# Kernel tuning notes

Measured on AMD Instinct MI355X. Metric: run time of the kernel, lower is better.

The kernel has to match this reference:

```python
import jax, jax.numpy as jnp
import numpy as np

L = 16          # num_sites
CHI_MAX = 64    # max bond dimension
VOCAB = 128000
TRUNC_EVERY = 10
DT = jnp.float32


def _mps_add(A, B):
    """Direct sum of two MPS (block-diagonal on bonds, boundaries concatenated)."""
    out = []
    for s in range(L):
        a, b = A[s], B[s]
        cla, d, cra = a.shape
        clb, _, crb = b.shape
        if s == 0:
            out.append(jnp.concatenate([a, b], axis=2))          # [1,d,cra+crb]
        elif s == L - 1:
            out.append(jnp.concatenate([a, b], axis=0))          # [cla+clb,d,1]
        else:
            t = jnp.zeros((cla + clb, d, cra + crb), a.dtype)
            t = t.at[:cla, :, :cra].set(a).at[cla:, :, cra:].set(b)
            out.append(t)
    return out


def _truncate(T, chi_max):
    """Left-to-right SVD sweep truncating every bond to <= chi_max."""
    T = list(T)
    for s in range(L - 1):
        cl, d, cr = T[s].shape
        U, S, Vh = jnp.linalg.svd(T[s].reshape(cl * d, cr), full_matrices=False)
        k = min(chi_max, int(S.shape[0]))
        T[s] = U[:, :k].reshape(cl, d, k)
        carry = S[:k, None] * Vh[:k]                              # [k, cr]
        T[s + 1] = jnp.einsum('kl,ldr->kdr', carry, T[s + 1])
    return T


def _forward(cores_hidden, cores_input, head_w, head_b, init_ctx, toks):
    # D=1 MPO core -> per-site 2x2 matrix acting on the physical index
    Wh = cores_hidden[:, 0, :, :, 0]   # [L,2,2]
    Wi = cores_input[:, 0, :, :, 0]    # [L,2,2]
    e0 = jnp.array([1.0, 0.0], DT).reshape(1, 2, 1)
    e1 = jnp.array([0.0, 1.0], DT).reshape(1, 2, 1)
    ctx = [init_ctx[s] for s in range(L)]
    for t, tok in enumerate(toks, start=1):
        bits = [(tok >> i) & 1 for i in range(L)]
        emb = [e1 if b else e0 for b in reversed(bits)]
        # h_{t+1} = W_hidden @ h_t  (+)  W_input @ embed(token)
        h = [jnp.einsum('ij,ljr->lir', Wh[s], ctx[s]) for s in range(L)]
        x = [jnp.einsum('ij,ljr->lir', Wi[s], emb[s]) for s in range(L)]
        ctx = _mps_add(h, x)
        if t % TRUNC_EVERY == 0 and ctx[0].shape[2] > CHI_MAX:
            ctx = _truncate(ctx, CHI_MAX)
    # predict(): mean of middle site over (left bond, phys) -> feature vector
    vec = ctx[L // 2].mean(axis=(0, 1))
    c = vec.shape[0]
    vec = jnp.pad(vec, (0, CHI_MAX - c)) if c < CHI_MAX else vec[:CHI_MAX]
    return head_w @ vec + head_b


def setup_inputs() -> dict:
    key = jax.random.key(0)
    k1, k2, k3, k4, k5, k6 = jax.random.split(key, 6)
    eye = jnp.eye(2, dtype=DT)
    cores_hidden = (0.02 * jax.random.normal(k1, (L, 1, 2, 2, 1), DT)).at[:, 0, :, :, 0].add(eye)
    cores_input = (0.02 * jax.random.normal(k2, (L, 1, 2, 2, 1), DT)).at[:, 0, :, :, 0].add(eye)
    head_w = jax.random.normal(k3, (VOCAB, CHI_MAX), DT) / jnp.sqrt(jnp.float32(CHI_MAX))
    head_b = 0.02 * jax.random.normal(k4, (VOCAB,), DT)
    init_ctx = jax.random.normal(k5, (L, 1, 2, 1), DT)
    token_ids = jax.random.randint(k6, (100,), 0, 65536, dtype=jnp.int32)
    return {"cores_hidden": cores_hidden, "cores_input": cores_input,
            "head_w": head_w, "head_b": head_b,
            "init_ctx": init_ctx, "token_ids": token_ids}


def reference(cores_hidden, cores_input, head_w, head_b, init_ctx, token_ids):
    toks = [int(t) for t in np.asarray(token_ids)]
    return _forward(cores_hidden, cores_input, head_w, head_b, init_ctx, toks)
```

## Files before the change

kernel.cpp:

```cpp
#include <hip/hip_runtime.h>

typedef double rl;
#define NT 256
#define NSV 71
#define LDA 128
#define LDV 72
#define SML 25
#define VOCAB 128000
#define LP 27
#define PB 129

#define EPS32 1.1920928955078125e-7
#define UNFL32 1.17549435e-38

#define O_CAR   0
#define O_COLS  4608
#define O_VEC   4800
#define O_MA    5120
#define O_MBLG  14208
#define O_MU    23552
#define O_MQ    32768
#define O_MVT   41984
#define O_SUB   47168
#define O_SVTB  52352
#define O_U2    57536
#define O_VT2   62720
#define O_QU    67904
#define O_QV    73088
#define O_TB    78272
#define O_D     83456
#define O_E     83528
#define O_TQ    83600
#define O_TP    83672

__device__ double g_ws[84000];

struct LeafCtx {
  rl LVT[26*LP], LU[26*LP];
  rl b1[26], b2[26], b3[26], b4[26];
  rl sc[6];
  int ia[26], ib[26], ic[26];
  int si[12];
};

struct Sh {
  rl d[72], e[72], tq[72], tp[72], rc[72], rs[72];
  rl dsig[72], zz[72], zh[72], sigm[72], vals[72];
  rl ta[72], tb[72];
  int srcU[72], srcVT[72], perm[72];
  int ia[72], ib[72], ic[72];
  int opk[12], opf[12], opa[12], opb[12], opq[12];
  rl sc[8];
  int si[16];
};

__device__ __forceinline__ void wsync(){
  asm volatile("s_waitcnt vmcnt(0) lgkmcnt(0)" ::: "memory");
}

__device__ __forceinline__ rl d_sign(rl a, rl b){ return (b >= 0.0) ? fabs(a) : -fabs(a); }
__device__ __forceinline__ rl dlapy2(rl x, rl y){
  rl ax=fabs(x), ay=fabs(y);
  rl w = ax>ay?ax:ay, z = ax>ay?ay:ax;
  if(z==0.0) return w;
  rl t = z/w; return w*sqrt(1.0+t*t);
}
__device__ void dlartg(rl f, rl g, rl* cs, rl* sn, rl* r){
  if(g==0.0){ *cs=1.0; *sn=0.0; *r=f; }
  else if(f==0.0){ *cs=0.0; *sn=d_sign(1.0,g); *r=fabs(g); }
  else{
    rl dd = sqrt(f*f+g*g);
    *cs = fabs(f)/dd;
    *r  = d_sign(dd, f);
    *sn = g/(*r);
  }
}

__device__ void dlas2(rl f, rl g, rl h, rl* ssmin, rl* ssmax){
  rl fa=fabs(f), ga=fabs(g), ha=fabs(h);
  rl fhmn=fmin(fa,ha), fhmx=fmax(fa,ha);
  if(fhmn==0.0){
    *ssmin=0.0;
    if(fhmx==0.0) *ssmax=ga;
    else { rl mx=fmax(fhmx,ga), mn=fmin(fhmx,ga); rl q=mn/mx; *ssmax=mx*sqrt(1.0+q*q); }
  } else {
    if(ga < fhmx){
      rl as=1.0+fhmn/fhmx, at=(fhmx-fhmn)/fhmx;
      rl au=(ga/fhmx); au=au*au;
      rl c=2.0/(sqrt(as*as+au)+sqrt(at*at+au));
      *ssmin=fhmn*c; *ssmax=fhmx/c;
    } else {
      rl au=fhmx/ga;
      if(au==0.0){ *ssmin=(fhmn*fhmx)/ga; *ssmax=ga; }
      else{
        rl as=1.0+fhmn/fhmx, at=(fhmx-fhmn)/fhmx;
        rl c=1.0/(sqrt(1.0+(as*au)*(as*au))+sqrt(1.0+(at*au)*(at*au)));
        *ssmin=(fhmn*c)*au; *ssmin=*ssmin+*ssmin;
        *ssmax=ga/(c+c);
      }
    }
  }
}

__device__ void dlasv2(rl f, rl g, rl h, rl* ssmin, rl* ssmax, rl* snr, rl* csr, rl* snl, rl* csl){
  rl ft=f, fa=fabs(f), ht=h, ha=fabs(h);
  int pmax=1;
  bool swp = (ha > fa);
  if(swp){ pmax=3; rl t=ft; ft=ht; ht=t; t=fa; fa=ha; ha=t; }
  rl gt=g, ga=fabs(g);
  rl clt=0, crt=0, slt=0, srt=0;
  if(ga==0.0){ *ssmin=ha; *ssmax=fa; clt=1.0; crt=1.0; slt=0.0; srt=0.0; }
  else{
    bool gasmal=true;
    if(ga > fa){
      pmax=2;
      if((fa/ga) < EPS32){
        gasmal=false;
        *ssmax=ga;
        if(ha>1.0) *ssmin=fa/(ga/ha); else *ssmin=(fa/ga)*ha;
        clt=1.0; slt=ht/gt; srt=1.0; crt=ft/gt;
      }
    }
    if(gasmal){
      rl dd=fa-ha;
      rl lv = (dd==fa) ? 1.0 : dd/fa;
      rl mq = gt/ft;
      rl tv = 2.0-lv;
      rl mm = mq*mq, tt = tv*tv;
      rl sv = sqrt(tt+mm);
      rl rv = (lv==0.0) ? fabs(mq) : sqrt(lv*lv+mm);
      rl a = 0.5*(sv+rv);
      *ssmin = ha/a; *ssmax = fa*a;
      rl t3;
      if(mm==0.0){
        if(lv==0.0) t3 = d_sign(2.0, ft)*d_sign(1.0, gt);
        else t3 = gt/d_sign(dd, ft) + mq/tv;
// ... 345 lines not shown

__device__ void leaf_exec(int f, int n, int sqre, int wantU, LeafCtx* lc, Sh* sh, int lane){
  rl* SVTB = g_ws + O_SVTB; rl* SUB = g_ws + O_SUB;
  int np = n + sqre;
  for(int w=lane; w<np*np; w+=64){ int r2=w/np, c=w-r2*np; lc->LVT[r2*LP+c]=SVTB[(f+r2)+(size_t)LDV*(f+c)]; }
  if(wantU) for(int w=lane; w<n*n; w+=64){ int r2=w/n, c=w-r2*n; lc->LU[r2*LP+c]=SUB[(f+r2)+(size_t)LDV*(f+c)]; }
  wsync();
  if(sqre==1){
    if(lane==0){
      rl cs,snv,rv; rl* dd=sh->d+f; rl* ee=sh->e+f;
      for(int i=0;i<n;++i){
        dlartg(dd[i],ee[i],&cs,&snv,&rv);
        dd[i]=rv;
        if(i<n-1){ ee[i]=snv*dd[i+1]; dd[i+1]=cs*dd[i+1]; }
        else ee[i]=0.0;
        lc->b1[i]=cs; lc->b2[i]=snv;
      }
    }
    wsync();
    if(lane<np){
      rl cur = lc->LVT[0*LP+lane];
      for(int j=0;j<n;++j){
        rl cj=lc->b1[j], sj=lc->b2[j];
        rl t=lc->LVT[(j+1)*LP+lane];
        lc->LVT[j*LP+lane] = sj*t + cj*cur;
        cur = cj*t - sj*cur;
      }
      lc->LVT[n*LP+lane] = cur;
    }
    wsync();
    if(lane==0){
      rl cs,snv,rv; rl* dd=sh->d+f; rl* ee=sh->e+f;
      for(int i=0;i<n-1;++i){
        dlartg(dd[i],ee[i],&cs,&snv,&rv);
        dd[i]=rv; ee[i]=snv*dd[i+1]; dd[i+1]=cs*dd[i+1];
        lc->b1[i]=cs; lc->b2[i]=snv;
      }
    }
    wsync();
    if(wantU && lane<n){
      rl cur = lc->LU[lane*LP+0];
      for(int j=0;j<n-1;++j){
        rl cj=lc->b1[j], sj=lc->b2[j];
        rl t=lc->LU[lane*LP+(j+1)];
        lc->LU[lane*LP+j] = sj*t + cj*cur;
        cur = cj*t - sj*cur;
      }
      lc->LU[lane*LP+(n-1)] = cur;
    }
    wsync();
  }
  bdsqr_wave(n, sh->d+f, sh->e+f, np, wantU? n:0, lc, lane);
  for(int w=lane; w<np*np; w+=64){ int r2=w/np, c=w-r2*np; SVTB[(f+r2)+(size_t)LDV*(f+c)]=lc->LVT[r2*LP+c]; }
  if(wantU) for(int w=lane; w<n*n; w+=64){ int r2=w/n, c=w-r2*n; SUB[(f+r2)+(size_t)LDV*(f+c)]=lc->LU[r2*LP+c]; }
}

__device__ void build_ops(int n, Sh* sh, int tid){
  if(tid==0){
    int sf[12], sn2[12], sq[12], sv[12]; int sp=0, no=0;
    sf[0]=0; sn2[0]=n; sq[0]=0; sv[0]=0; sp=1;
    while(sp>0){
      --sp;
      int f=sf[sp], nn=sn2[sp], q=sq[sp], v=sv[sp];
      if(nn<=SML){ sh->opk[no]=0; sh->opf[no]=f; sh->opa[no]=nn; sh->opb[no]=0; sh->opq[no]=q; ++no; }
      else if(v==0){
        int nl=nn/2, nr=nn-nl-1;
        sf[sp]=f; sn2[sp]=nn; sq[sp]=q; sv[sp]=1; ++sp;
        sf[sp]=f+nl+1; sn2[sp]=nr; sq[sp]=q; sv[sp]=0; ++sp;
        sf[sp]=f; sn2[sp]=nl; sq[sp]=1; sv[sp]=0; ++sp;
      } else {
        int nl=nn/2, nr=nn-nl-1;
        sh->opk[no]=1; sh->opf[no]=f; sh->opa[no]=nl; sh->opb[no]=nr; sh->opq[no]=q; ++no;
      }
    }
    int tk[12], tf2[12], ta2[12], tb3[12], tq3[12]; int c=0;
    for(int i=0;i<no;++i) if(sh->opk[i]==0){ tk[c]=0; tf2[c]=sh->opf[i]; ta2[c]=sh->opa[i]; tb3[c]=sh->opb[i]; tq3[c]=sh->opq[i]; ++c; }
    for(int i=0;i<no;++i) if(sh->opk[i]==1){ tk[c]=1; tf2[c]=sh->opf[i]; ta2[c]=sh->opa[i]; tb3[c]=sh->opb[i]; tq3[c]=sh->opq[i]; ++c; }
    for(int i=0;i<no;++i){ sh->opk[i]=tk[i]; sh->opf[i]=tf2[i]; sh->opa[i]=ta2[i]; sh->opb[i]=tb3[i]; sh->opq[i]=tq3[i]; }
    sh->si[6]=no;
  }
  __syncthreads();
}

__device__ void lasd1_merge(int f, int nl, int nr, int sqre, int wantU, rl* QV, Sh* sh, int tid){
  rl* SUB = g_ws + O_SUB; rl* SVTB = g_ws + O_SVTB;
  rl* U2 = g_ws + O_U2; rl* VT2 = g_ws + O_VT2; rl* QU = g_ws + O_QU;
  int n = nl+nr+1, m = n+sqre;
  {
    rl alpha = sh->d[f+nl], beta = sh->e[f+nl];
    if(tid==0){
      sh->sc[0]=alpha; sh->sc[1]=beta;
      sh->vals[0]=0.0;
      sh->zz[0] = alpha*SVTB[(f+nl)+(size_t)LDV*(f+nl)];
      sh->srcU[0]=-1; sh->srcVT[0]=f+nl;
    } else if(tid<n){
      int i=tid;
      if(i<=nl){
        sh->vals[i]=sh->d[f+i-1];
        sh->zz[i]=alpha*SVTB[(f+i-1)+(size_t)LDV*(f+nl)];
        sh->srcU[i]=f+i-1; sh->srcVT[i]=f+i-1;
      } else {
        int j=i-1-nl;
        sh->vals[i]=sh->d[f+nl+1+j];
        sh->zz[i]=beta*SVTB[(f+nl+1+j)+(size_t)LDV*(f+nl+1)];
        sh->srcU[i]=f+nl+1+j; sh->srcVT[i]=f+nl+1+j;
      }
    }
  }
  __syncthreads();
  if(sqre==1){
    if(tid==0){
      rl zM = sh->sc[1]*SVTB[(f+n)+(size_t)LDV*(f+nl+1)];
      rl c,s2,r2;
      dlartg(sh->zz[0], zM, &c, &s2, &r2);
      sh->zz[0]=r2; sh->sc[2]=c; sh->sc[3]=s2;
    }
    __syncthreads();
    rl c=sh->sc[2], s=sh->sc[3];
    int ra=f+nl, rb=f+n;
    for(int k=tid;k<m;k+=NT){
      size_t ci=(size_t)LDV*(f+k);
      rl a=SVTB[ra+ci], b=SVTB[rb+ci];
      SVTB[ra+ci]=c*a+s*b; SVTB[rb+ci]=-s*a+c*b;
    }
  }
  __syncthreads();
  {
    rl lm = (tid<n)? fabs(sh->vals[tid]) : 0.0;
    for(int off=32;off>0;off>>=1) lm = fmax(lm, __shfl_xor(lm,off,64));
    if((tid&63)==0) sh->ta[tid>>6]=lm;
  }
  __syncthreads();
  {
    rl maxd = fmax(fmax(sh->ta[0],sh->ta[1]), fmax(sh->ta[2],sh->ta[3]));
    rl tol = 8.0*EPS32*fmax(maxd, fmax(fabs(sh->sc[0]), fabs(sh->sc[1])));
    if(tid>=1 && tid<n){
      bool ndt = fabs(sh->zz[tid])>tol;
      rl vt = sh->vals[tid];
      int rank=0, Kc=0;
      for(int j=1;j<n;++j){
        bool ndj = fabs(sh->zz[j])>tol;
        if(ndj) ++Kc;
        if(ndj==ndt){
          rl vj=sh->vals[j];
          if(vj<vt || (vj==vt && j<tid)) ++rank;
        }
      }
      int pos = ndt ? (1+rank) : (1+Kc+rank);
      sh->ic[pos]=tid;
    }
    if(tid==0){
      int Kc=0;
      for(int j=1;j<n;++j) if(fabs(sh->zz[j])>tol) ++Kc;
      sh->ic[0]=0;
      sh->si[0]=1+Kc; sh->si[1]=n; sh->si[2]=m; sh->si[3]=f; sh->si[4]=nl;
    }
  }
  __syncthreads();
  int K=sh->si[0], n_=sh->si[1], m_=sh->si[2], f_=sh->si[3], nl_=sh->si[4];
  if(tid<n_){ sh->ta[tid]=sh->vals[tid]; sh->tb[tid]=sh->zz[tid]; sh->ia[tid]=sh->srcU[tid]; sh->ib[tid]=sh->srcVT[tid]; }
  __syncthreads();
  if(tid<n_){
    int p=sh->ic[tid];
    sh->dsig[tid]=sh->ta[p]; sh->zz[tid]=sh->tb[p]; sh->srcU[tid]=sh->ia[p]; sh->srcVT[tid]=sh->ib[p];
  }
  __syncthreads();
  if(tid==0){
    rl rho=0.0; for(int t=0;t<K;++t){ rl zv=sh->zz[t]; rho += zv*zv; }
    sh->sc[4]=rho;
  }
  if(wantU){
    for(int w=tid; w<n_*n_; w+=NT){
      int col=w/n_, row=w-col*n_;
      int su=sh->srcU[col];
      rl v;
      if(su<0) v = (row==nl_) ? 1.0 : 0.0;
      else v = SUB[(f_+row)+(size_t)LDV*su];
      U2[row+(size_t)LDV*col]=v;
    }
  }
  for(int w=tid; w<n_*m_; w+=NT){
    int row=w/m_, col=w-row*m_;
    VT2[row+(size_t)LDV*col] = SVTB[sh->srcVT[row]+(size_t)LDV*(f_+col)];
  }
  __syncthreads();
  rl rho=sh->sc[4];
  for(int j=tid;j<K;j+=NT){
    rl lo=sh->dsig[j];
    rl hi=(j<K-1)? sh->dsig[j+1] : sqrt(sh->dsig[K-1]*sh->dsig[K-1]+rho);
    for(int it=0; it<130; ++it){
      rl mid=0.5*(lo+hi);
      if(mid<=lo || mid>=hi) break;
      rl g=1.0;
      for(int i2=0;i2<K;++i2){
        rl zi=sh->zz[i2];
        g += zi*zi/((sh->dsig[i2]-mid)*(sh->dsig[i2]+mid));
      }
      if(g<0.0) lo=mid; else hi=mid;
    }
    sh->sigm[j]=0.5*(lo+hi);
  }
  __syncthreads();
  for(int i2=tid;i2<K;i2+=NT){
    rl di=sh->dsig[i2];
    rl p=(di - sh->sigm[K-1])*(di + sh->sigm[K-1]);
    for(int j=0;j<i2;++j)
      p *= (di - sh->sigm[j])*(di + sh->sigm[j])/((di - sh->dsig[j])*(di + sh->dsig[j]));
    for(int j=i2;j<K-1;++j)
      p *= (di - sh->sigm[j])*(di + sh->sigm[j])/((di - sh->dsig[j+1])*(di + sh->dsig[j+1]));
    sh->zh[i2] = d_sign(sqrt(fabs(p)), sh->zz[i2]);
  }
  __syncthreads();
  for(int j=tid;j<K;j+=NT){
    rl sj=sh->sigm[j];
    rl nu=0.0, nv=0.0;
    for(int i2=0;i2<K;++i2){
      rl di=sh->dsig[i2];
      rl vv=sh->zh[i2]/((di-sj)*(di+sj));
      QV[i2+(size_t)LDV*j]=vv; nv+=vv*vv;
      if(wantU){
        rl uu=(i2==0)? -1.0 : di*vv;
        QU[i2+(size_t)LDV*j]=uu; nu+=uu*uu;
      }
    }
    nv=1.0/sqrt(nv);
    for(int i2=0;i2<K;++i2) QV[i2+(size_t)LDV*j]*=nv;
    if(wantU){
      nu=1.0/sqrt(nu);
      for(int i2=0;i2<K;++i2) QU[i2+(size_t)LDV*j]*=nu;
    }
  }
  __syncthreads();
  if(tid==0){
    int nd2=n_-K;
    for(int t=0;t<nd2;++t) sh->ia[t]=K+t;
    int ps=K-1, pd=nd2-1;
    int t=0;
    while(t<n_){
      rl vs = (ps>=0)? sh->sigm[ps] : -1.0;
      rl vd = (pd>=0)? sh->dsig[sh->ia[pd]] : -1.0;
      if(vs >= vd){ sh->perm[t]=ps; sh->vals[t]=vs; --ps; }
      else { sh->perm[t]=1000+sh->ia[pd]; sh->vals[t]=vd; --pd; }
      ++t;
    }
  }
  __syncthreads();
  if(tid<n_) sh->d[f_+tid]=sh->vals[tid];
  if(wantU){
    for(int w=tid; w<n_*n_; w+=NT){
      int t=w/n_, row=w-t*n_;
      int src=sh->perm[t];
      rl acc;
      if(src>=1000) acc = U2[row+(size_t)LDV*(src-1000)];
      else{
        const rl* urow = U2 + row;
        const rl* qcol = QU + (size_t)LDV*src;
        rl s=0.0; int i=0;
        for(; i+16<=K; i+=16){
          rl a[16], b[16];
          #pragma unroll
          for(int u=0;u<16;++u){ a[u]=urow[(size_t)LDV*(size_t)(i+u)]; b[u]=qcol[i+u]; }
          #pragma unroll
          for(int u=0;u<16;++u) s += a[u]*b[u];
        }
        for(; i<K; ++i) s += urow[(size_t)LDV*i]*qcol[i];
        acc=s;
      }
      SUB[(f_+row)+(size_t)LDV*(f_+t)] = acc;
    }
  }
  for(int w=tid; w<n_*m_; w+=NT){
    int t=w/m_, col=w-t*m_;
    int src=sh->perm[t];
    rl acc;
    if(src>=1000) acc = VT2[(src-1000)+(size_t)LDV*col];
    else{
      const rl* qcol = QV + (size_t)LDV*src;
      const rl* vcol = VT2 + (size_t)LDV*col;
      rl s=0.0; int i=0;
      for(; i+16<=K; i+=16){
        rl a[16], b[16];
        #pragma unroll
        for(int u=0;u<16;++u){ a[u]=qcol[i+u]; b[u]=vcol[i+u]; }
        #pragma unroll
        for(int u=0;u<16;++u) s += a[u]*b[u];
      }
      for(; i<K; ++i) s += qcol[i]*vcol[i];
      acc=s;
    }
    SVTB[(f_+t)+(size_t)LDV*(f_+col)] = acc;
  }
  __syncthreads();
}

__device__ __forceinline__ void gebd2_upper(rl* A, int ld, int m, int n, Sh* sh, int tid){
  const int lane = tid & 63;
  rl pend_scl = 0.0; int pend_ds = 0;
  for(int i=0;i<n;++i){
    rl ps=0.0;
    for(int r=i+1+lane;r<m;r+=64){ rl vv=A[r+(size_t)ld*i]; ps+=vv*vv; }
    for(int off=32;off>0;off>>=1) ps += __shfl_xor(ps,off,64);
    rl alpha=A[i+(size_t)ld*i];
    rl xn=sqrt(ps);
    rl beta,tau,scl; int ds;
    if(xn==0.0){ tau=0.0; beta=alpha; scl=0.0; ds=0; }
    else{ beta=-d_sign(dlapy2(alpha,xn),alpha); tau=(beta-alpha)/beta; scl=1.0/(alpha-beta); ds=1; }
    if(tid==0){ sh->d[i]=beta; sh->tq[i]=tau; }
    if(tau!=0.0)
      app_left_s(A, ld, i, m, i+1, n, A+(size_t)ld*i, scl, tau, tid);
    if(pend_ds && tid>=128){
      int c = i+1 + (tid-128);
      if(c < n) A[(i-1)+(size_t)ld*c] *= pend_scl;
    }
    __syncthreads();
    if(i<n-1){
      rl ps2=0.0;
      for(int c=i+2+lane;c<n;c+=64){ rl vv=A[i+(size_t)ld*c]; ps2+=vv*vv; }
      for(int off=32;off>0;off>>=1) ps2 += __shfl_xor(ps2,off,64);
      rl alpha2=A[i+(size_t)ld*(i+1)];
      rl xn2=sqrt(ps2);
      rl beta2,tau2,scl2; int ds2;
      if(xn2==0.0){ tau2=0.0; beta2=alpha2; scl2=0.0; ds2=0; }
      else{ beta2=-d_sign(dlapy2(alpha2,xn2),alpha2); tau2=(beta2-alpha2)/beta2; scl2=1.0/(alpha2-beta2); ds2=1; }
      if(tid==0){ sh->e[i]=beta2; sh->tp[i]=tau2; }
      if(tau2!=0.0)
        app_right_s(A, ld, i+1, m, i+1, n, A+i, ld, scl2, tau2, tid);
      if(ds && tid>=128){
        int r = i+1 + (tid-128);
        if(r < m) A[r+(size_t)ld*i] *= scl;
      }
      pend_ds = ds2; pend_scl = scl2;
      __syncthreads();
    } else {
      if(tid==0) sh->tp[i]=0.0;
      __syncthreads();
      if(ds) for(int r=i+1+tid; r<m; r+=NT) A[r+(size_t)ld*(n-1)] *= scl;
      __syncthreads();
    }
  }
}

__device__ __forceinline__ void gebd2_lower(rl* A, int ld, int m, int n, Sh* sh, int tid){
  const int lane = tid & 63;
  rl pend_scl = 0.0; int pend_ds = 0;
  int last_ds = 0; rl last_scl = 0.0;
  for(int i=0;i<m;++i){
    rl ps=0.0;
    for(int c=i+1+lane;c<n;c+=64){ rl vv=A[i+(size_t)ld*c]; ps+=vv*vv; }
    for(int off=32;off>0;off>>=1) ps += __shfl_xor(ps,off,64);
    rl alpha=A[i+(size_t)ld*i];
    rl xn=sqrt(ps);
    rl beta,tau,scl; int ds;
    if(xn==0.0){ tau=0.0; beta=alpha; scl=0.0; ds=0; }
    else{ beta=-d_sign(dlapy2(alpha,xn),alpha); tau=(beta-alpha)/beta; scl=1.0/(alpha-beta); ds=1; }
    if(tid==0){ sh->d[i]=beta; sh->tp[i]=tau; }
    if(tau!=0.0)
      app_right_s(A, ld, i+1, m, i, n, A+i, ld, scl, tau, tid);
    if(pend_ds && tid>=128){
      int r = i+1 + (tid-128);
      if(r < m) A[r+(size_t)ld*(i-1)] *= pend_scl;
    }
    __syncthreads();
    if(i<m-1){
      rl ps2=0.0;
      for(int r=i+2+lane;r<m;r+=64){ rl vv=A[r+(size_t)ld*i]; ps2+=vv*vv; }
      for(int off=32;off>0;off>>=1) ps2 += __shfl_xor(ps2,off,64);
      rl alpha2=A[(i+1)+(size_t)ld*i];
      rl xn2=sqrt(ps2);
      rl beta2,tau2,scl2; int ds2;
      if(xn2==0.0){ tau2=0.0; beta2=alpha2; scl2=0.0; ds2=0; }
      else{ beta2=-d_sign(dlapy2(alpha2,xn2),alpha2); tau2=(beta2-alpha2)/beta2; scl2=1.0/(alpha2-beta2); ds2=1; }
      if(tid==0){ sh->e[i]=beta2; sh->tq[i]=tau2; }
      if(tau2!=0.0)
        app_left_s(A, ld, i+1, m, i+1, n, A+(size_t)ld*i, scl2, tau2, tid);
      if(ds && tid>=128){
        int c = i+1 + (tid-128);
        if(c < n) A[i+(size_t)ld*c] *= scl;
      }
      pend_ds = ds2; pend_scl = scl2;
      __syncthreads();
    } else {
      last_ds = ds; last_scl = scl;
      __syncthreads();
      if(last_ds) for(int c=i+1+tid; c<n; c+=NT) A[(m-1)+(size_t)ld*c] *= last_scl;
      __syncthreads();
    }
  }
}

__device__ __forceinline__ void gelq2(rl* A, int ld, int m, int n, Sh* sh, int tid){
  const int lane = tid & 63;
  rl pend_scl=0.0, pend_beta=0.0; int pend_ds=0;
  for(int i=0;i<m;++i){
    rl ps=0.0;
    for(int c=i+1+lane;c<n;c+=64){ rl vv=A[i+(size_t)ld*c]; ps+=vv*vv; }
    for(int off=32;off>0;off>>=1) ps += __shfl_xor(ps,off,64);
    rl alpha=A[i+(size_t)ld*i];
    rl xn=sqrt(ps);
    rl beta,tau,scl; int ds;
    if(xn==0.0){ tau=0.0; beta=alpha; scl=0.0; ds=0; }
    else{ beta=-d_sign(dlapy2(alpha,xn),alpha); tau=(beta-alpha)/beta; scl=1.0/(alpha-beta); ds=1; }
    if(tid==0) sh->rs[i]=tau;
    if(i<m-1 && tau!=0.0)
      app_right_s(A, ld, i+1, m, i, n, A+i, ld, scl, tau, tid);
    if(i>0 && tid>=128){
      if(pend_ds){ int c = i + (tid-128); if(c<n) A[(i-1)+(size_t)ld*c] *= pend_scl; }
      if(tid==128) A[(i-1)+(size_t)ld*(i-1)] = pend_beta;
    }
    pend_ds=ds; pend_scl=scl; pend_beta=beta;
    __syncthreads();
  }
  if(tid>=128){
    if(pend_ds){ int c = m + (tid-128); if(c<n) A[(m-1)+(size_t)ld*c] *= pend_scl; }
    if(tid==128) A[(m-1)+(size_t)ld*(m-1)] = pend_beta;
  }
  __syncthreads();
}


__global__ __launch_bounds__(NT)
void k_bidiag(const float* __restrict__ ch, const float* __restrict__ ci,
              const float* __restrict__ ictx, const int* __restrict__ tok,
              int s, int m)
{
  __shared__ Sh sh;
  extern __shared__ rl MBL[];
  int tid = threadIdx.x;
  rl* MA = g_ws + O_MA; rl* MQ = g_ws + O_MQ; rl* TB = g_ws + O_TB;
  if(tid==0){
    rl W00=ch[s*4+0], W01=ch[s*4+1], W10=ch[s*4+2], W11=ch[s*4+3];
    rl P00=1,P01=0,P10=0,P11=1;
    for(int mexp=0;mexp<=70;++mexp){
      int j=70-mexp;
      rl v0,v1;
      if(j==0){ v0=ictx[s*2+0]; v1=ictx[s*2+1]; }
      else{
        int b=(tok[j-1]>>(15-s))&1;
        v0=ci[s*4+b]; v1=ci[s*4+2+b];
      }
      g_ws[O_COLS + 0 + 2*j] = P00*v0+P01*v1;
      g_ws[O_COLS + 1 + 2*j] = P10*v0+P11*v1;
      rl n00=W00*P00+W01*P10, n01=W00*P01+W01*P11;
      rl n10=W10*P00+W11*P10, n11=W10*P01+W11*P11;
      P00=n00;P01=n01;P10=n10;P11=n11;
    }
  }
  __syncthreads();
  for(int w=tid; w<m*NSV; w+=NT){
    int j=w/m, r2=w-j*m;
    int l=r2>>1, dd2=r2&1;
    rl cv = g_ws[O_COLS + dd2 + 2*j];
    MA[r2+(size_t)LDA*j] = (s==0)? cv : g_ws[O_CAR + l + 64*j]*cv;
  }
  __syncthreads();
  if(m==128){
    for(int w=tid;w<128*NSV;w+=NT){ int c=w>>7, r2=w&127; MBL[r2+(size_t)PB*c]=MA[r2+(size_t)LDA*c]; }
    __syncthreads();
    gebd2_upper(MBL, PB, 128, NSV, &sh, tid);
    for(int w=tid;w<PB*NSV;w+=NT) g_ws[O_MBLG+w]=MBL[w];
  } else if(m==64){
    for(int w=tid;w<64*NSV;w+=NT){ int c=w>>6, r2=w&63; MBL[r2+(size_t)PB*c]=MA[r2+(size_t)LDA*c]; }
    __syncthreads();
    gebd2_lower(MBL, PB, 64, NSV, &sh, tid);
    for(int w=tid;w<PB*NSV;w+=NT) g_ws[O_MBLG+w]=MBL[w];
  } else {
    for(int w=tid;w<m*NSV;w+=NT){ int c=w/m, r2=w-c*m; MBL[r2+(size_t)PB*c]=MA[r2+(size_t)LDA*c]; }
    __syncthreads();
    gelq2(MBL, PB, m, NSV, &sh, tid);
    for(int w=tid;w<m*NSV;w+=NT){ int c=w/m, r2=w-c*m; MQ[r2+(size_t)LDA*c]=(r2==c)?1.0:0.0; }
    __syncthreads();
    if(tid<m){
      int r=tid;
      for(int j=m-1;j>=0;--j){
        rl tau=sh.rs[j];
        if(tau!=0.0) row_apply(MQ + r + (size_t)LDA*j, LDA, MBL + j + (size_t)PB*(j+1), PB, NSV-j-1, tau);
      }
    }
    __syncthreads();
    for(int w=tid;w<m*m;w+=NT){ int c=w/m, r2=w-c*m; TB[r2+(size_t)LDV*c]=(r2>=c)? MBL[r2+(size_t)PB*c]:0.0; }
    __syncthreads();
    gebd2_upper(TB, LDV, m, m, &sh, tid);
  }
  if(tid<72){
    g_ws[O_D+tid]=sh.d[tid]; g_ws[O_E+tid]=sh.e[tid];
    g_ws[O_TQ+tid]=sh.tq[tid]; g_ws[O_TP+tid]=sh.tp[tid];
  }
}

__global__ __launch_bounds__(NT)
void k_leaf(int s, int m)
{
  __shared__ Sh sh;
  __shared__ LeafCtx lct[4];
  int tid = threadIdx.x;
  if(tid<72){ sh.d[tid]=g_ws[O_D+tid]; sh.e[tid]=g_ws[O_E+tid]; }
  __syncthreads();
  int wantU = (s==8)?1:0;
  int n_eff = (m==128)? NSV : m;
  if(m==64){
    if(tid==0){
      for(int i=0;i<63;++i){
        rl cs,snv,rv;
        dlartg(sh.d[i], sh.e[i], &cs,&snv,&rv);
        sh.d[i]=rv; sh.e[i]=snv*sh.d[i+1]; sh.d[i+1]=cs*sh.d[i+1];
      }
    }
    __syncthreads();
  }
  rl* SUB = g_ws + O_SUB; rl* SVTB = g_ws + O_SVTB;
  for(int w=tid; w<LDV*LDV; w+=NT){
    int c=w/LDV, r2=w-c*LDV; rl v=(r2==c)?1.0:0.0;
    SVTB[w]=v;
    if(wantU) SUB[w]=v;
  }
  __syncthreads();
  if(n_eff<=SML){
    if((tid>>6)==0) leaf_exec(0, n_eff, 0, wantU, &lct[0], &sh, tid&63);
    __syncthreads();
  } else {
    build_ops(n_eff, &sh, tid);
    int no=sh.si[6];
    int o=0;
    while(o<no && sh.opk[o]==0){
      int cnt=1;
      while(o+cnt<no && sh.opk[o+cnt]==0 && cnt<4) ++cnt;
      int wid = tid>>6;
      if(wid<cnt) leaf_exec(sh.opf[o+wid], sh.opa[o+wid], sh.opq[o+wid], wantU, &lct[wid], &sh, tid&63);
      __syncthreads();
      o += cnt;
    }
  }
  if(tid<72){ g_ws[O_D+tid]=sh.d[tid]; g_ws[O_E+tid]=sh.e[tid]; }
}

__global__ __launch_bounds__(NT)
void k_merge(int s, int m)
{
  __shared__ Sh sh;
  __shared__ rl QV[(size_t)LDV*71];
  int tid = threadIdx.x;
  if(tid<72){ sh.d[tid]=g_ws[O_D+tid]; sh.e[tid]=g_ws[O_E+tid]; }
  __syncthreads();
  int wantU = (s==8)?1:0;
  int n_eff = (m==128)? NSV : m;
  if(n_eff>SML){
    build_ops(n_eff, &sh, tid);
    int no=sh.si[6];
    for(int o=0;o<no;++o){
      if(sh.opk[o]==1)
        lasd1_merge(sh.opf[o], sh.opa[o], sh.opb[o], sh.opq[o], wantU, QV, &sh, tid);
    }
  }
  __syncthreads();
  if(tid<72) g_ws[O_D+tid]=sh.d[tid];
}

__global__ __launch_bounds__(NT)
void k_post(const float* __restrict__ ch, int s, int m)
{
  __shared__ Sh sh;
  extern __shared__ rl MBL[];
  int tid = threadIdx.x;
  rl* MU=g_ws+O_MU; rl* MVT=g_ws+O_MVT; rl* MQ=g_ws+O_MQ;
  rl* SUB=g_ws+O_SUB; rl* SVTB=g_ws+O_SVTB; rl* TB=g_ws+O_TB; rl* VT2=g_ws+O_VT2;
  if(tid<72){
    sh.d[tid]=g_ws[O_D+tid];
    sh.tq[tid]=g_ws[O_TQ+tid];
    sh.tp[tid]=g_ws[O_TP+tid];
  }
  __syncthreads();
  int k = (m<64)? m : 64;
  if(m==128){
    if(s==8){
      for(int w=tid;w<128*NSV;w+=NT){ int c=w>>7, r2=w&127; MU[r2+(size_t)LDA*c]=(r2<NSV)? SUB[r2+(size_t)LDV*c]:0.0; }
      for(int w=tid;w<PB*NSV;w+=NT) MBL[w]=g_ws[O_MBLG+w];
      __syncthreads();
      if(tid<NSV){
        int c=tid;
        rl* colb = MU + (size_t)LDA*c;
        for(int i=NSV-1;i>=0;--i){
          rl tau=sh.tq[i];
          if(tau!=0.0) row_apply(colb+i, 1, MBL + (size_t)PB*i + i + 1, 1, 128-i-1, tau);
        }
      }
      __syncthreads();
      if(tid==0){
        rl W00=ch[8*4+0], W01=ch[8*4+1], W10=ch[8*4+2], W11=ch[8*4+3];
        rl P00=1,P01=0,P10=0,P11=1;
        for(int it=0;it<30;++it){
          rl n00=W00*P00+W01*P10, n01=W00*P01+W01*P11;
          rl n10=W10*P00+W11*P10, n11=W10*P01+W11*P11;
          P00=n00;P01=n01;P10=n10;P11=n11;
        }
        sh.sc[0]=P00+P10; sh.sc[1]=P01+P11;
      }
      __syncthreads();
      for(int r2=tid; r2<64; r2+=NT){
        rl acc=0.0;
        for(int l=0;l<64;++l)
          acc += sh.sc[0]*MU[(2*l)+(size_t)LDA*r2] + sh.sc[1]*MU[(2*l+1)+(size_t)LDA*r2];
        g_ws[O_VEC + r2] = acc/188.0;
      }
    } else {
      for(int w=tid;w<LDV*NSV;w+=NT) MVT[w]=SVTB[w];
      for(int w=tid;w<PB*NSV;w+=NT) MBL[w]=g_ws[O_MBLG+w];
      __syncthreads();
      if(tid<NSV){
        int r=tid;
        for(int i=NSV-2;i>=0;--i){
          rl tau=sh.tp[i];
          if(tau!=0.0) row_apply(MVT + r + (size_t)LDV*(i+1), LDV, MBL + i + (size_t)PB*(i+2), PB, NSV-i-2, tau);
        }
      }
      __syncthreads();
      for(int w=tid; w<k*NSV; w+=NT){
        int j=w/k, l=w-j*k;
        g_ws[O_CAR + l + 64*j] = sh.d[l]*MVT[l+(size_t)LDV*j];
      }
    }
  } else if(m==64){
    for(int w=tid;w<64*NSV;w+=NT){ int c=w>>6, r2=w&63; MVT[r2+(size_t)LDV*c]=(c<64)? SVTB[r2+(size_t)LDV*c]:0.0; }
    for(int w=tid;w<PB*NSV;w+=NT) MBL[w]=g_ws[O_MBLG+w];
    __syncthreads();
    if(tid<64){
      int r=tid;
      for(int i=63;i>=0;--i){
        rl tau=sh.tp[i];
        if(tau!=0.0) row_apply(MVT + r + (size_t)LDV*i, LDV, MBL + i + (size_t)PB*(i+1), PB, NSV-i-1, tau);
      }
    }
    __syncthreads();
    for(int w=tid; w<k*NSV; w+=NT){
      int j=w/k, l=w-j*k;
      g_ws[O_CAR + l + 64*j] = sh.d[l]*MVT[l+(size_t)LDV*j];
    }
  } else {
    for(int w=tid;w<m*m;w+=NT){ int c=w/m, r2=w-c*m; VT2[r2+(size_t)LDV*c]=SVTB[r2+(size_t)LDV*c]; }
    __syncthreads();
    if(tid<m){
      int r=tid;
      for(int i=m-2;i>=0;--i){
        rl tau=sh.tp[i];
        if(tau!=0.0) row_apply(VT2 + r + (size_t)LDV*(i+1), LDV, TB + i + (size_t)LDV*(i+2), LDV, m-i-2, tau);
      }
    }
    __syncthreads();
    for(int w=tid;w<m*NSV;w+=NT){
      int c=w/m, r2=w-c*m;
      const rl* vrow = VT2 + r2;
      const rl* qcol = MQ + (size_t)LDA*c;
      rl s2=0.0; int t=0;
      for(; t+16<=m; t+=16){
        rl a[16], b[16];
        #pragma unroll
        for(int u=0;u<16;++u){ a[u]=vrow[(size_t)LDV*(size_t)(t+u)]; b[u]=qcol[t+u]; }
        #pragma unroll
        for(int u=0;u<16;++u) s2 += a[u]*b[u];
      }
      for(; t+4<=m; t+=4){
        rl a0=vrow[(size_t)LDV*t], a1=vrow[(size_t)LDV*(t+1)], a2=vrow[(size_t)LDV*(t+2)], a3=vrow[(size_t)LDV*(t+3)];
        rl b0=qcol[t], b1=qcol[t+1], b2=qcol[t+2], b3=qcol[t+3];
        s2+=a0*b0; s2+=a1*b1; s2+=a2*b2; s2+=a3*b3;
      }
      for(; t<m; ++t) s2 += vrow[(size_t)LDV*t]*qcol[t];
      MVT[r2+(size_t)LDV*c]=s2;
    }
    __syncthreads();
    for(int w=tid; w<k*NSV; w+=NT){
      int j=w/k, l=w-j*k;
      g_ws[O_CAR + l + 64*j] = sh.d[l]*MVT[l+(size_t)LDV*j];
    }
  }
}

__global__ __launch_bounds__(NT)
void head_kernel(const float* __restrict__ hw, const float* __restrict__ hb,
                 float* __restrict__ out)
{
  __shared__ float v[64];
  int tid=threadIdx.x;
  if(tid<64) v[tid]=(float)g_ws[O_VEC + tid];
  __syncthreads();
  int i = blockIdx.x*NT + tid;
  if(i<VOCAB){
    const float4* row = (const float4*)(hw + (size_t)i*64);
    float acc=0.f;
    #pragma unroll
    for(int c4=0;c4<16;++c4){
      float4 r4=row[c4];
      acc += r4.x*v[4*c4] + r4.y*v[4*c4+1] + r4.z*v[4*c4+2] + r4.w*v[4*c4+3];
    }
    out[i]=acc+hb[i];
  }
}

extern "C" void kernel_launch(void* const* d_in, const int* in_sizes, int n_in,
                              void* d_out, int out_size, void* d_ws, size_t ws_size,
                              hipStream_t stream)
{
  const float* ch  = (const float*)d_in[0];
  const float* ci  = (const float*)d_in[1];
  const float* hw  = (const float*)d_in[2];
  const float* hb  = (const float*)d_in[3];
  const float* ict = (const float*)d_in[4];
  const int*   tk  = (const int*)d_in[5];
  (void)d_ws; (void)ws_size; (void)in_sizes; (void)n_in; (void)out_size;

  static const int ms[9] = {2,4,8,16,32,64,128,128,128};
  size_t dynls = (size_t)PB*NSV*sizeof(double);
  for(int s=0;s<9;++s){
    hipLaunchKernelGGL(k_bidiag, dim3(1), dim3(NT), dynls, stream, ch, ci, ict, tk, s, ms[s]);
    hipLaunchKernelGGL(k_leaf,   dim3(1), dim3(NT), 0,     stream, s, ms[s]);
    if(ms[s] >= 32)
      hipLaunchKernelGGL(k_merge, dim3(1), dim3(NT), 0,    stream, s, ms[s]);
    hipLaunchKernelGGL(k_post,   dim3(1), dim3(NT), dynls, stream, ch, s, ms[s]);
  }
  hipLaunchKernelGGL(head_kernel, dim3((VOCAB+NT-1)/NT), dim3(NT), 0, stream,
                     hw, hb, (float*)d_out);
}
```

Measured before the change: 8.123 ms.

## Fuse SVD stage kernels and run sibling divide-and-conquer merges concurrently

Merges the bidiagonalization and leaf-solve kernels into one, and the merge and post-processing kernels into another, so each truncation step needs two launches instead of four and passes less state through global memory. When the merge tree has three merge operations, the two independent sibling merges now run at the same time on two 128-thread halves of the block, using offset shared and workspace regions. The final merge then runs on the full block. The risks are higher shared-memory use per kernel (LeafCtx and QV now live alongside the dynamic buffer) and correctness hazards if the per-half offsets overlap in the U2/VT2/QU workspaces.

```diff
diff --git a/kernel.cpp b/kernel.cpp
--- a/kernel.cpp
+++ b/kernel.cpp
@@ -50,8 +50,8 @@
   int srcU[72], srcVT[72], perm[72];
   int ia[72], ib[72], ic[72];
   int opk[12], opf[12], opa[12], opb[12], opq[12];
-  rl sc[8];
-  int si[16];
+  rl sc[16];
+  int si[24];
 };
 
 __device__ __forceinline__ void wsync(){
@@ -563,179 +563,184 @@
   __syncthreads();
 }
 
-__device__ void lasd1_merge(int f, int nl, int nr, int sqre, int wantU, rl* QV, Sh* sh, int tid){
+__device__ void lasd1_merge2(int f, int nl, int nr, int sqre, int wantU,
+                             rl* QVL, int qofs, int base, Sh* sh, int ltid, int lnt){
   rl* SUB = g_ws + O_SUB; rl* SVTB = g_ws + O_SVTB;
   rl* U2 = g_ws + O_U2; rl* VT2 = g_ws + O_VT2; rl* QU = g_ws + O_QU;
+  rl* sc = sh->sc + (base?8:0);
+  int* si = sh->si + (base?16:0);
   int n = nl+nr+1, m = n+sqre;
   {
     rl alpha = sh->d[f+nl], beta = sh->e[f+nl];
-    if(tid==0){
-      sh->sc[0]=alpha; sh->sc[1]=beta;
-      sh->vals[0]=0.0;
-      sh->zz[0] = alpha*SVTB[(f+nl)+(size_t)LDV*(f+nl)];
-      sh->srcU[0]=-1; sh->srcVT[0]=f+nl;
-    } else if(tid<n){
-      int i=tid;
+    if(ltid==0){
+      sc[0]=alpha; sc[1]=beta;
+      sh->vals[base]=0.0;
+      sh->zz[base] = alpha*SVTB[(f+nl)+(size_t)LDV*(f+nl)];
+      sh->srcU[base]=-1; sh->srcVT[base]=f+nl;
+    } else if(ltid<n){
+      int i=ltid;
       if(i<=nl){
-        sh->vals[i]=sh->d[f+i-1];
-        sh->zz[i]=alpha*SVTB[(f+i-1)+(size_t)LDV*(f+nl)];
-        sh->srcU[i]=f+i-1; sh->srcVT[i]=f+i-1;
+        sh->vals[base+i]=sh->d[f+i-1];
+        sh->zz[base+i]=alpha*SVTB[(f+i-1)+(size_t)LDV*(f+nl)];
+        sh->srcU[base+i]=f+i-1; sh->srcVT[base+i]=f+i-1;
       } else {
         int j=i-1-nl;
-        sh->vals[i]=sh->d[f+nl+1+j];
-        sh->zz[i]=beta*SVTB[(f+nl+1+j)+(size_t)LDV*(f+nl+1)];
-        sh->srcU[i]=f+nl+1+j; sh->srcVT[i]=f+nl+1+j;
-      }
-    }
+        sh->vals[base+i]=sh->d[f+nl+1+j];
+        sh->zz[base+i]=beta*SVTB[(f+nl+1+j)+(size_t)LDV*(f+nl+1)];
+        sh->srcU[base+i]=f+nl+1+j; sh->srcVT[base+i]=f+nl+1+j;
+      }
+    }
+  }
+  __syncthreads();
+  if(ltid==0 && sqre==1){
+    rl zM = sc[1]*SVTB[(f+n)+(size_t)LDV*(f+nl+1)];
+    rl c,s2,r2;
+    dlartg(sh->zz[base], zM, &c, &s2, &r2);
+    sh->zz[base]=r2; sc[2]=c; sc[3]=s2;
   }
   __syncthreads();
   if(sqre==1){
-    if(tid==0){
-      rl zM = sh->sc[1]*SVTB[(f+n)+(size_t)LDV*(f+nl+1)];
-      rl c,s2,r2;
-      dlartg(sh->zz[0], zM, &c, &s2, &r2);
-      sh->zz[0]=r2; sh->sc[2]=c; sh->sc[3]=s2;
-    }
-    __syncthreads();
-    rl c=sh->sc[2], s=sh->sc[3];
+    rl c=sc[2], s=sc[3];
     int ra=f+nl, rb=f+n;
-    for(int k=tid;k<m;k+=NT){
+    for(int k=ltid;k<m;k+=lnt){
       size_t ci=(size_t)LDV*(f+k);
       rl a=SVTB[ra+ci], b=SVTB[rb+ci];
       SVTB[ra+ci]=c*a+s*b; SVTB[rb+ci]=-s*a+c*b;
     }
   }
   __syncthreads();
+  if(ltid==0){
+    rl maxd=0.0; for(int i=0;i<n;++i) maxd=fmax(maxd,fabs(sh->vals[base+i]));
+    rl tol = 8.0*EPS32*fmax(maxd, fmax(fabs(sc[0]), fabs(sc[1])));
+    sc[5]=tol;
+    int Kc=0;
+    for(int j=1;j<n;++j) if(fabs(sh->zz[base+j]) > tol) ++Kc;
+    sh->ic[base]=0;
+    si[0]=1+Kc; si[1]=n; si[2]=m; si[3]=f; si[4]=nl;
+  }
+  __syncthreads();
   {
-    rl lm = (tid<n)? fabs(sh->vals[tid]) : 0.0;
-    for(int off=32;off>0;off>>=1) lm = fmax(lm, __shfl_xor(lm,off,64));
-    if((tid&63)==0) sh->ta[tid>>6]=lm;
-  }
-  __syncthreads();
-  {
-    rl maxd = fmax(fmax(sh->ta[0],sh->ta[1]), fmax(sh->ta[2],sh->ta[3]));
-    rl tol = 8.0*EPS32*fmax(maxd, fmax(fabs(sh->sc[0]), fabs(sh->sc[1])));
-    if(tid>=1 && tid<n){
-      bool ndt = fabs(sh->zz[tid])>tol;
-      rl vt = sh->vals[tid];
+    rl tol=sc[5];
+    if(ltid>=1 && ltid<n){
+      bool ndt = fabs(sh->zz[base+ltid])>tol;
+      rl vt = sh->vals[base+ltid];
       int rank=0, Kc=0;
       for(int j=1;j<n;++j){
-        bool ndj = fabs(sh->zz[j])>tol;
+        bool ndj = fabs(sh->zz[base+j])>tol;
         if(ndj) ++Kc;
         if(ndj==ndt){
-          rl vj=sh->vals[j];
-          if(vj<vt || (vj==vt && j<tid)) ++rank;
+          rl vj=sh->vals[base+j];
+          if(vj<vt || (vj==vt && j<ltid)) ++rank;
         }
       }
       int pos = ndt ? (1+rank) : (1+Kc+rank);
-      sh->ic[pos]=tid;
-    }
-    if(tid==0){
-      int Kc=0;
-      for(int j=1;j<n;++j) if(fabs(sh->zz[j])>tol) ++Kc;
-      sh->ic[0]=0;
-      sh->si[0]=1+Kc; sh->si[1]=n; sh->si[2]=m; sh->si[3]=f; sh->si[4]=nl;
-    }
-  }
-  __syncthreads();
-  int K=sh->si[0], n_=sh->si[1], m_=sh->si[2], f_=sh->si[3], nl_=sh->si[4];
-  if(tid<n_){ sh->ta[tid]=sh->vals[tid]; sh->tb[tid]=sh->zz[tid]; sh->ia[tid]=sh->srcU[tid]; sh->ib[tid]=sh->srcVT[tid]; }
-  __syncthreads();
-  if(tid<n_){
-    int p=sh->ic[tid];
-    sh->dsig[tid]=sh->ta[p]; sh->zz[tid]=sh->tb[p]; sh->srcU[tid]=sh->ia[p]; sh->srcVT[tid]=sh->ib[p];
-  }
-  __syncthreads();
-  if(tid==0){
-    rl rho=0.0; for(int t=0;t<K;++t){ rl zv=sh->zz[t]; rho += zv*zv; }
-    sh->sc[4]=rho;
+      sh->ic[base+pos]=ltid;
+    }
+  }
+  __syncthreads();
+  int K=si[0], n_=si[1], m_=si[2], f_=si[3], nl_=si[4];
+  if(ltid<n_){ sh->ta[base+ltid]=sh->vals[base+ltid]; sh->tb[base+ltid]=sh->zz[base+ltid]; sh->ia[base+ltid]=sh->srcU[base+ltid]; sh->ib[base+ltid]=sh->srcVT[base+ltid]; }
+  __syncthreads();
+  if(ltid<n_){
+    int p=sh->ic[base+ltid];
+    sh->dsig[base+ltid]=sh->ta[base+p]; sh->zz[base+ltid]=sh->tb[base+p]; sh->srcU[base+ltid]=sh->ia[base+p]; sh->srcVT[base+ltid]=sh->ib[base+p];
+  }
+  __syncthreads();
+  if(ltid==0){
+    rl rho=0.0; for(int t=0;t<K;++t){ rl zv=sh->zz[base+t]; rho += zv*zv; }
+    sc[4]=rho;
   }
   if(wantU){
-    for(int w=tid; w<n_*n_; w+=NT){
+    for(int w=ltid; w<n_*n_; w+=lnt){
       int col=w/n_, row=w-col*n_;
-      int su=sh->srcU[col];
+      int su=sh->srcU[base+col];
       rl v;
       if(su<0) v = (row==nl_) ? 1.0 : 0.0;
       else v = SUB[(f_+row)+(size_t)LDV*su];
-      U2[row+(size_t)LDV*col]=v;
-    }
-  }
-  for(int w=tid; w<n_*m_; w+=NT){
+      U2[(base+row)+(size_t)LDV*(base+col)]=v;
+    }
+  }
+  for(int w=ltid; w<n_*m_; w+=lnt){
     int row=w/m_, col=w-row*m_;
-    VT2[row+(size_t)LDV*col] = SVTB[sh->srcVT[row]+(size_t)LDV*(f_+col)];
-  }
-  __syncthreads();
-  rl rho=sh->sc[4];
-  for(int j=tid;j<K;j+=NT){
-    rl lo=sh->dsig[j];
-    rl hi=(j<K-1)? sh->dsig[j+1] : sqrt(sh->dsig[K-1]*sh->dsig[K-1]+rho);
-    for(int it=0; it<130; ++it){
-      rl mid=0.5*(lo+hi);
-      if(mid<=lo || mid>=hi) break;
-      rl g=1.0;
-      for(int i2=0;i2<K;++i2){
-        rl zi=sh->zz[i2];
-        g += zi*zi/((sh->dsig[i2]-mid)*(sh->dsig[i2]+mid));
-      }
-      if(g<0.0) lo=mid; else hi=mid;
-    }
-    sh->sigm[j]=0.5*(lo+hi);
-  }
-  __syncthreads();
-  for(int i2=tid;i2<K;i2+=NT){
-    rl di=sh->dsig[i2];
-    rl p=(di - sh->sigm[K-1])*(di + sh->sigm[K-1]);
+    VT2[(base+row)+(size_t)LDV*(base+col)] = SVTB[sh->srcVT[base+row]+(size_t)LDV*(f_+col)];
+  }
+  __syncthreads();
+  {
+    rl rho=sc[4];
+    if(ltid<K){
+      int j=ltid;
+      rl lo=sh->dsig[base+j];
+      rl hi=(j<K-1)? sh->dsig[base+j+1] : sqrt(sh->dsig[base+K-1]*sh->dsig[base+K-1]+rho);
+      for(int it=0; it<130; ++it){
+        rl mid=0.5*(lo+hi);
+        if(mid<=lo || mid>=hi) break;
+        rl g=1.0;
+        for(int i2=0;i2<K;++i2){
+          rl zi=sh->zz[base+i2];
+          g += zi*zi/((sh->dsig[base+i2]-mid)*(sh->dsig[base+i2]+mid));
+        }
+        if(g<0.0) lo=mid; else hi=mid;
+      }
+      sh->sigm[base+j]=0.5*(lo+hi);
+    }
+  }
+  __syncthreads();
+  if(ltid<K){
+    int i2=ltid;
+    rl di=sh->dsig[base+i2];
+    rl p=(di - sh->sigm[base+K-1])*(di + sh->sigm[base+K-1]);
     for(int j=0;j<i2;++j)
-      p *= (di - sh->sigm[j])*(di + sh->sigm[j])/((di - sh->dsig[j])*(di + sh->dsig[j]));
+      p *= (di - sh->sigm[base+j])*(di + sh->sigm[base+j])/((di - sh->dsig[base+j])*(di + sh->dsig[base+j]));
     for(int j=i2;j<K-1;++j)
-      p *= (di - sh->sigm[j])*(di + sh->sigm[j])/((di - sh->dsig[j+1])*(di + sh->dsig[j+1]));
-    sh->zh[i2] = d_sign(sqrt(fabs(p)), sh->zz[i2]);
-  }
-  __syncthreads();
-  for(int j=tid;j<K;j+=NT){
-    rl sj=sh->sigm[j];
+      p *= (di - sh->sigm[base+j])*(di + sh->sigm[base+j])/((di - sh->dsig[base+j+1])*(di + sh->dsig[base+j+1]));
+    sh->zh[base+i2] = d_sign(sqrt(fabs(p)), sh->zz[base+i2]);
+  }
+  __syncthreads();
+  if(ltid<K){
+    int j=ltid;
+    rl sj=sh->sigm[base+j];
     rl nu=0.0, nv=0.0;
     for(int i2=0;i2<K;++i2){
-      rl di=sh->dsig[i2];
-      rl vv=sh->zh[i2]/((di-sj)*(di+sj));
-      QV[i2+(size_t)LDV*j]=vv; nv+=vv*vv;
+      rl di=sh->dsig[base+i2];
+      rl vv=sh->zh[base+i2]/((di-sj)*(di+sj));
+      QVL[i2+(size_t)LDV*(j+qofs)]=vv; nv+=vv*vv;
       if(wantU){
         rl uu=(i2==0)? -1.0 : di*vv;
-        QU[i2+(size_t)LDV*j]=uu; nu+=uu*uu;
+        QU[i2+(size_t)LDV*(j+qofs)]=uu; nu+=uu*uu;
       }
     }
     nv=1.0/sqrt(nv);
-    for(int i2=0;i2<K;++i2) QV[i2+(size_t)LDV*j]*=nv;
+    for(int i2=0;i2<K;++i2) QVL[i2+(size_t)LDV*(j+qofs)]*=nv;
     if(wantU){
       nu=1.0/sqrt(nu);
-      for(int i2=0;i2<K;++i2) QU[i2+(size_t)LDV*j]*=nu;
-    }
-  }
-  __syncthreads();
-  if(tid==0){
+      for(int i2=0;i2<K;++i2) QU[i2+(size_t)LDV*(j+qofs)]*=nu;
+    }
+  }
+  __syncthreads();
+  if(ltid==0){
     int nd2=n_-K;
-    for(int t=0;t<nd2;++t) sh->ia[t]=K+t;
+    for(int t=0;t<nd2;++t) sh->ia[base+t]=K+t;
     int ps=K-1, pd=nd2-1;
     int t=0;
     while(t<n_){
-      rl vs = (ps>=0)? sh->sigm[ps] : -1.0;
-      rl vd = (pd>=0)? sh->dsig[sh->ia[pd]] : -1.0;
-      if(vs >= vd){ sh->perm[t]=ps; sh->vals[t]=vs; --ps; }
-      else { sh->perm[t]=1000+sh->ia[pd]; sh->vals[t]=vd; --pd; }
+      rl vs = (ps>=0)? sh->sigm[base+ps] : -1.0;
+      rl vd = (pd>=0)? sh->dsig[base+sh->ia[base+pd]] : -1.0;
+      if(vs >= vd){ sh->perm[base+t]=ps; sh->vals[base+t]=vs; --ps; }
+      else { sh->perm[base+t]=1000+sh->ia[base+pd]; sh->vals[base+t]=vd; --pd; }
       ++t;
     }
   }
   __syncthreads();
-  if(tid<n_) sh->d[f_+tid]=sh->vals[tid];
+  if(ltid<n_) sh->d[f_+ltid]=sh->vals[base+ltid];
   if(wantU){
-    for(int w=tid; w<n_*n_; w+=NT){
+    for(int w=ltid; w<n_*n_; w+=lnt){
       int t=w/n_, row=w-t*n_;
-      int src=sh->perm[t];
+      int src=sh->perm[base+t];
       rl acc;
-      if(src>=1000) acc = U2[row+(size_t)LDV*(src-1000)];
+      if(src>=1000) acc = U2[(base+row)+(size_t)LDV*(base+(src-1000))];
       else{
-        const rl* urow = U2 + row;
-        const rl* qcol = QU + (size_t)LDV*src;
+        const rl* urow = U2 + (base+row) + (size_t)LDV*base;
+        const rl* qcol = QU + (size_t)LDV*(src+qofs);
         rl s=0.0; int i=0;
         for(; i+16<=K; i+=16){
           rl a[16], b[16];
@@ -750,14 +755,14 @@
       SUB[(f_+row)+(size_t)LDV*(f_+t)] = acc;
     }
   }
-  for(int w=tid; w<n_*m_; w+=NT){
+  for(int w=ltid; w<n_*m_; w+=lnt){
     int t=w/m_, col=w-t*m_;
-    int src=sh->perm[t];
+    int src=sh->perm[base+t];
     rl acc;
-    if(src>=1000) acc = VT2[(src-1000)+(size_t)LDV*col];
+    if(src>=1000) acc = VT2[(base+(src-1000))+(size_t)LDV*(base+col)];
     else{
-      const rl* qcol = QV + (size_t)LDV*src;
-      const rl* vcol = VT2 + (size_t)LDV*col;
+      const rl* qcol = QVL + (size_t)LDV*(src+qofs);
+      const rl* vcol = VT2 + base + (size_t)LDV*(base+col);
       rl s=0.0; int i=0;
       for(; i+16<=K; i+=16){
         rl a[16], b[16];
@@ -898,13 +903,13 @@
   __syncthreads();
 }
 
-
 __global__ __launch_bounds__(NT)
-void k_bidiag(const float* __restrict__ ch, const float* __restrict__ ci,
-              const float* __restrict__ ictx, const int* __restrict__ tok,
-              int s, int m)
+void k_front(const float* __restrict__ ch, const float* __restrict__ ci,
+             const float* __restrict__ ictx, const int* __restrict__ tok,
+             int s, int m)
 {
   __shared__ Sh sh;
+  __shared__ LeafCtx lct[4];
   extern __shared__ rl MBL[];
   int tid = threadIdx.x;
   rl* MA = g_ws + O_MA; rl* MQ = g_ws + O_MQ; rl* TB = g_ws + O_TB;
@@ -944,6 +949,14 @@
     __syncthreads();
     gebd2_lower(MBL, PB, 64, NSV, &sh, tid);
     for(int w=tid;w<PB*NSV;w+=NT) g_ws[O_MBLG+w]=MBL[w];
+    __syncthreads();
+    if(tid==0){
+      for(int i=0;i<63;++i){
+        rl cs,snv,rv;
+        dlartg(sh.d[i], sh.e[i], &cs,&snv,&rv);
+        sh.d[i]=rv; sh.e[i]=snv*sh.d[i+1]; sh.d[i+1]=cs*sh.d[i+1];
+      }
+    }
   } else {
     for(int w=tid;w<m*NSV;w+=NT){ int c=w/m, r2=w-c*m; MBL[r2+(size_t)PB*c]=MA[r2+(size_t)LDA*c]; }
     __syncthreads();
@@ -962,32 +975,9 @@
     __syncthreads();
     gebd2_upper(TB, LDV, m, m, &sh, tid);
   }
-  if(tid<72){
-    g_ws[O_D+tid]=sh.d[tid]; g_ws[O_E+tid]=sh.e[tid];
-    g_ws[O_TQ+tid]=sh.tq[tid]; g_ws[O_TP+tid]=sh.tp[tid];
-  }
-}
-
-__global__ __launch_bounds__(NT)
-void k_leaf(int s, int m)
-{
-  __shared__ Sh sh;
-  __shared__ LeafCtx lct[4];
-  int tid = threadIdx.x;
-  if(tid<72){ sh.d[tid]=g_ws[O_D+tid]; sh.e[tid]=g_ws[O_E+tid]; }
   __syncthreads();
   int wantU = (s==8)?1:0;
   int n_eff = (m==128)? NSV : m;
-  if(m==64){
-    if(tid==0){
-      for(int i=0;i<63;++i){
-        rl cs,snv,rv;
-        dlartg(sh.d[i], sh.e[i], &cs,&snv,&rv);
-        sh.d[i]=rv; sh.e[i]=snv*sh.d[i+1]; sh.d[i+1]=cs*sh.d[i+1];
-      }
-    }
-    __syncthreads();
-  }
   rl* SUB = g_ws + O_SUB; rl* SVTB = g_ws + O_SVTB;
   for(int w=tid; w<LDV*LDV; w+=NT){
     int c=w/LDV, r2=w-c*LDV; rl v=(r2==c)?1.0:0.0;
@@ -1011,43 +1001,46 @@
       o += cnt;
     }
   }
-  if(tid<72){ g_ws[O_D+tid]=sh.d[tid]; g_ws[O_E+tid]=sh.e[tid]; }
+  if(tid<72){
+    g_ws[O_D+tid]=sh.d[tid]; g_ws[O_E+tid]=sh.e[tid];
+    g_ws[O_TQ+tid]=sh.tq[tid]; g_ws[O_TP+tid]=sh.tp[tid];
+  }
 }
 
 __global__ __launch_bounds__(NT)
-void k_merge(int s, int m)
+void k_back(const float* __restrict__ ch, int s, int m)
 {
   __shared__ Sh sh;
-  __shared__ rl QV[(size_t)LDV*71];
-  int tid = threadIdx.x;
-  if(tid<72){ sh.d[tid]=g_ws[O_D+tid]; sh.e[tid]=g_ws[O_E+tid]; }
-  __syncthreads();
-  int wantU = (s==8)?1:0;
-  int n_eff = (m==128)? NSV : m;
-  if(n_eff>SML){
-    build_ops(n_eff, &sh, tid);
-    int no=sh.si[6];
-    for(int o=0;o<no;++o){
-      if(sh.opk[o]==1)
-        lasd1_merge(sh.opf[o], sh.opa[o], sh.opb[o], sh.opq[o], wantU, QV, &sh, tid);
-    }
-  }
-  __syncthreads();
-  if(tid<72) g_ws[O_D+tid]=sh.d[tid];
-}
-
-__global__ __launch_bounds__(NT)
-void k_post(const float* __restrict__ ch, int s, int m)
-{
-  __shared__ Sh sh;
+  __shared__ rl QV[(size_t)LDV*72];
   extern __shared__ rl MBL[];
   int tid = threadIdx.x;
   rl* MU=g_ws+O_MU; rl* MVT=g_ws+O_MVT; rl* MQ=g_ws+O_MQ;
   rl* SUB=g_ws+O_SUB; rl* SVTB=g_ws+O_SVTB; rl* TB=g_ws+O_TB; rl* VT2=g_ws+O_VT2;
   if(tid<72){
-    sh.d[tid]=g_ws[O_D+tid];
-    sh.tq[tid]=g_ws[O_TQ+tid];
-    sh.tp[tid]=g_ws[O_TP+tid];
+    sh.d[tid]=g_ws[O_D+tid]; sh.e[tid]=g_ws[O_E+tid];
+    sh.tq[tid]=g_ws[O_TQ+tid]; sh.tp[tid]=g_ws[O_TP+tid];
+  }
+  __syncthreads();
+  int wantU = (s==8)?1:0;
+  int n_eff = (m==128)? NSV : m;
+  if(n_eff > SML){
+    build_ops(n_eff, &sh, tid);
+    int no=sh.si[6];
+    int mstart=0; while(mstart<no && sh.opk[mstart]==0) ++mstart;
+    int nm = no - mstart;
+    if(nm==3){
+      int slot = tid>>7, ltid = tid&127;
+      int o = mstart + slot;
+      lasd1_merge2(sh.opf[o], sh.opa[o], sh.opb[o], sh.opq[o], wantU,
+                   QV, 36*slot, 36*slot, &sh, ltid, 128);
+      int r = mstart+2;
+      lasd1_merge2(sh.opf[r], sh.opa[r], sh.opb[r], sh.opq[r], wantU,
+                   QV, 0, 0, &sh, tid, NT);
+    } else {
+      for(int o=mstart;o<no;++o)
+        lasd1_merge2(sh.opf[o], sh.opa[o], sh.opb[o], sh.opq[o], wantU,
+                     QV, 0, 0, &sh, tid, NT);
+    }
   }
   __syncthreads();
   int k = (m<64)? m : 64;
@@ -1190,11 +1183,8 @@
   static const int ms[9] = {2,4,8,16,32,64,128,128,128};
   size_t dynls = (size_t)PB*NSV*sizeof(double);
   for(int s=0;s<9;++s){
-    hipLaunchKernelGGL(k_bidiag, dim3(1), dim3(NT), dynls, stream, ch, ci, ict, tk, s, ms[s]);
-    hipLaunchKernelGGL(k_leaf,   dim3(1), dim3(NT), 0,     stream, s, ms[s]);
-    if(ms[s] >= 32)
-      hipLaunchKernelGGL(k_merge, dim3(1), dim3(NT), 0,    stream, s, ms[s]);
-    hipLaunchKernelGGL(k_post,   dim3(1), dim3(NT), dynls, stream, ch, s, ms[s]);
+    hipLaunchKernelGGL(k_front, dim3(1), dim3(NT), dynls, stream, ch, ci, ict, tk, s, ms[s]);
+    hipLaunchKernelGGL(k_back,  dim3(1), dim3(NT), dynls, stream, ch, s, ms[s]);
   }
   hipLaunchKernelGGL(head_kernel, dim3((VOCAB+NT-1)/NT), dim3(NT), 0, stream,
                      hw, hb, (float*)d_out);
```

After: 7.319 ms. -9.9%, faster.
